# Kernel optimization log

Measured on AMD Instinct MI355X. Metric: run time of the kernel, lower is better.

The kernel has to match this reference:

```python
import jax, jax.numpy as jnp
import numpy as np

THETA = jnp.array([1.0, -0.5, 0.25, -0.125, 0.0625], dtype=jnp.float32)
N_NODES = 100000
N_EDGES = 1600000
D_FEAT = 32


def setup_inputs() -> dict:
    key = jax.random.key(0)
    k1, k2, k3 = jax.random.split(key, 3)
    feat = jax.random.normal(k1, (N_NODES, D_FEAT), dtype=jnp.float32)
    src = jax.random.randint(k2, (N_EDGES,), 0, N_NODES, dtype=jnp.int64)
    dst = jax.random.randint(k3, (N_EDGES,), 0, N_NODES, dtype=jnp.int64)
    return {"feat": feat, "src": src, "dst": dst}


def reference(feat, src, dst):
    n = feat.shape[0]
    # in-degree per node (edges counted by destination), clamped to >= 1
    deg = jax.ops.segment_sum(jnp.ones(src.shape[0], dtype=feat.dtype), dst, num_segments=n)
    d_invsqrt = jnp.maximum(deg, 1.0) ** -0.5  # [N]
    d_invsqrt = d_invsqrt[:, None]             # [N, 1]

    def unn_laplacian(f):
        # f - D^-1/2 A D^-1/2 f, via gather-from-src, scatter-sum-to-dst
        scaled = f * d_invsqrt                                   # [N, d]
        agg = jax.ops.segment_sum(scaled[src], dst, num_segments=n)  # [N, d]
        return f - agg * d_invsqrt

    h = THETA[0] * feat
    f = feat
    for k in range(1, THETA.shape[0]):
        f = unn_laplacian(f)
        h = h + THETA[k] * f
    return h
```

## Files before the change

### kernel.cpp

```cpp
#include <hip/hip_runtime.h>
#include <hip/hip_fp16.h>

#define D 32
#define BSHIFT 8
#define BNODES 256
#define NB_MAX 512
#define CHUNK 4096
#define CTHREADS 512

union H8 {
    float4 f4;
    __half2 h2[4];
};

__global__ void cursor_init(int* __restrict__ bcursor, int nb, int cap) {
    int tid = threadIdx.x;
    if (tid < nb) bcursor[tid] = tid * cap;
}

__global__ void scatter_bucket(const int* __restrict__ src, const int* __restrict__ dst,
                               int* __restrict__ bcursor, unsigned int* __restrict__ staged,
                               int n_edges, int cap) {
    __shared__ int cnt[NB_MAX];
    __shared__ int sbase[NB_MAX];
    __shared__ int gbase[NB_MAX];
    __shared__ unsigned int stg[CHUNK];
    __shared__ unsigned short stgb[CHUNK];
    int tid = threadIdx.x;
    for (int j = tid; j < NB_MAX; j += CTHREADS) cnt[j] = 0;
    __syncthreads();
    int base = blockIdx.x * CHUNK;
    const int EPT = CHUNK / CTHREADS;
    int b8[EPT], r8[EPT], s8[EPT], d8[EPT];
    #pragma unroll
    for (int k = 0; k < EPT; ++k) {
        int i = base + k * CTHREADS + tid;
        if (i < n_edges) {
            int dv = dst[i];
            s8[k] = src[i];
            d8[k] = dv & (BNODES - 1);
            b8[k] = dv >> BSHIFT;
            r8[k] = atomicAdd(&cnt[b8[k]], 1);
        } else {
            b8[k] = -1;
        }
    }
    __syncthreads();
    int v = cnt[tid];
    sbase[tid] = v;
    __syncthreads();
    for (int off = 1; off < NB_MAX; off <<= 1) {
        int t = (tid >= off) ? sbase[tid - off] : 0;
        __syncthreads();
        sbase[tid] += t;
        __syncthreads();
    }
    int excl = sbase[tid] - v;
    __syncthreads();
    sbase[tid] = excl;
    gbase[tid] = v ? atomicAdd(&bcursor[tid], v) : 0;
    __syncthreads();
    #pragma unroll
    for (int k = 0; k < EPT; ++k) {
        if (b8[k] >= 0) {
            int p = sbase[b8[k]] + r8[k];
            stg[p] = ((unsigned)s8[k] << BSHIFT) | (unsigned)d8[k];
            stgb[p] = (unsigned short)b8[k];
        }
    }
    __syncthreads();
    int valid = n_edges - base;
    if (valid > CHUNK) valid = CHUNK;
    for (int j = tid; j < valid; j += CTHREADS) {
        int b = stgb[j];
        int idx = gbase[b] + (j - sbase[b]);
        if (idx < (b + 1) * cap)
            staged[idx] = stg[j];
    }
}

__global__ void bucket_finalize(const int* __restrict__ bcursor, const unsigned int* __restrict__ staged,
                                int cap, int* __restrict__ csr, int2* __restrict__ rowinfo,
                                float* __restrict__ dinv2, float* __restrict__ dsq,
                                const float* __restrict__ feat, __half* __restrict__ s0,
                                int n_nodes) {
    __shared__ int cnt[BNODES];
    __shared__ int scn[BNODES];
    __shared__ int cursor[BNODES];
    __shared__ float ldinv[BNODES];
    int tid = threadIdx.x;
    int b = blockIdx.x;
    int node0 = b << BSHIFT;
    int nn = n_nodes - node0;
    if (nn > BNODES) nn = BNODES;
    int base = b * cap;
    int m = bcursor[b] - base;
    if (m > cap) m = cap;
    if (tid < BNODES) cnt[tid] = 0;
    __syncthreads();
    for (int j = tid; j < m; j += CTHREADS)
        atomicAdd(&cnt[staged[base + j] & (BNODES - 1)], 1);
    __syncthreads();
    if (tid < BNODES) scn[tid] = cnt[tid];
    __syncthreads();
    for (int off = 1; off < BNODES; off <<= 1) {
        int t = 0;
        if (tid < BNODES && tid >= off) t = scn[tid - off];
        __syncthreads();
        if (tid < BNODES) scn[tid] += t;
        __syncthreads();
    }
    if (tid < BNODES) {
        int excl = scn[tid] - cnt[tid];
        cursor[tid] = excl;
        if (tid < nn) {
            int2 ri = {base + excl, base + excl + cnt[tid]};
            rowinfo[node0 + tid] = ri;
            float fd = (float)cnt[tid];
            fd = fd < 1.0f ? 1.0f : fd;
            float dn = rsqrtf(fd);
            ldinv[tid] = dn;
            dinv2[node0 + tid] = dn * dn;
            dsq[node0 + tid] = sqrtf(fd);
        }
    }
    __syncthreads();
    for (int j = tid; j < m; j += CTHREADS) {
        unsigned int p = staged[base + j];
        int d = p & (BNODES - 1);
        int pos = atomicAdd(&cursor[d], 1);
        csr[base + pos] = (int)(p >> BSHIFT);
    }
    int ntask = nn * 4;
    for (int t = tid; t < ntask; t += CTHREADS) {
        int nl = t >> 2;
        int q8 = (t & 3) << 3;
        float dn = ldinv[nl];
        size_t off = ((size_t)(node0 + nl) << 5) + q8;
        float4 a = *reinterpret_cast<const float4*>(&feat[off]);
        float4 bb = *reinterpret_cast<const float4*>(&feat[off + 4]);
        H8 o;
        o.h2[0] = __floats2half2_rn(a.x * dn, a.y * dn);
        o.h2[1] = __floats2half2_rn(a.z * dn, a.w * dn);
        o.h2[2] = __floats2half2_rn(bb.x * dn, bb.y * dn);
        o.h2[3] = __floats2half2_rn(bb.z * dn, bb.w * dn);
        *reinterpret_cast<float4*>(&s0[off]) = o.f4;
    }
}

__device__ __forceinline__ void acc_row(const __half* __restrict__ s_cur, int sn, int q8,
                                        float& a0, float& a1, float& a2, float& a3,
                                        float& a4, float& a5, float& a6, float& a7) {
    H8 u;
    u.f4 = *reinterpret_cast<const float4*>(&s_cur[((size_t)sn << 5) + q8]);
    float2 p0 = __half22float2(u.h2[0]);
    float2 p1 = __half22float2(u.h2[1]);
    float2 p2 = __half22float2(u.h2[2]);
    float2 p3 = __half22float2(u.h2[3]);
    a0 += p0.x; a1 += p0.y; a2 += p1.x; a3 += p1.y;
    a4 += p2.x; a5 += p2.y; a6 += p3.x; a7 += p3.y;
}

__global__ void hop_kernel(const int2* __restrict__ rowinfo, const int* __restrict__ csr,
                           const float* __restrict__ dinv2, const __half* __restrict__ s_cur,
                           __half* __restrict__ s_next, int n_nodes) {
    int t = blockIdx.x * blockDim.x + threadIdx.x;
    int node = t >> 2;
    if (node >= n_nodes) return;
    int q8 = (t & 3) << 3;
    int2 ri = rowinfo[node];
    int e = ri.x, end = ri.y;
    float a0 = 0.f, a1 = 0.f, a2 = 0.f, a3 = 0.f, a4 = 0.f, a5 = 0.f, a6 = 0.f, a7 = 0.f;
    for (; e + 3 < end; e += 4) {
        int s0 = csr[e], s1 = csr[e + 1], s2 = csr[e + 2], s3 = csr[e + 3];
        acc_row(s_cur, s0, q8, a0, a1, a2, a3, a4, a5, a6, a7);
        acc_row(s_cur, s1, q8, a0, a1, a2, a3, a4, a5, a6, a7);
        acc_row(s_cur, s2, q8, a0, a1, a2, a3, a4, a5, a6, a7);
        acc_row(s_cur, s3, q8, a0, a1, a2, a3, a4, a5, a6, a7);
    }
    for (; e < end; ++e)
        acc_row(s_cur, csr[e], q8, a0, a1, a2, a3, a4, a5, a6, a7);
    size_t off = ((size_t)node << 5) + q8;
    float dn2 = dinv2[node];
    H8 sc;
    sc.f4 = *reinterpret_cast<const float4*>(&s_cur[off]);
    float2 c0 = __half22float2(sc.h2[0]);
    float2 c1 = __half22float2(sc.h2[1]);
    float2 c2 = __half22float2(sc.h2[2]);
    float2 c3 = __half22float2(sc.h2[3]);
    H8 so;
    so.h2[0] = __floats2half2_rn(c0.x - a0 * dn2, c0.y - a1 * dn2);
    so.h2[1] = __floats2half2_rn(c1.x - a2 * dn2, c1.y - a3 * dn2);
    so.h2[2] = __floats2half2_rn(c2.x - a4 * dn2, c2.y - a5 * dn2);
    so.h2[3] = __floats2half2_rn(c3.x - a6 * dn2, c3.y - a7 * dn2);
    *reinterpret_cast<float4*>(&s_next[off]) = so.f4;
}

__global__ void hop_last_kernel(const int2* __restrict__ rowinfo, const int* __restrict__ csr,
                                const float* __restrict__ dinv2, const float* __restrict__ dsq,
                                const __half* __restrict__ s1, const __half* __restrict__ s2,
                                const __half* __restrict__ s3, const float* __restrict__ feat,
                                float* __restrict__ h, int n_nodes) {
    int t = blockIdx.x * blockDim.x + threadIdx.x;
    int node = t >> 2;
    if (node >= n_nodes) return;
    int q8 = (t & 3) << 3;
    int2 ri = rowinfo[node];
    int e = ri.x, end = ri.y;
    float a0 = 0.f, a1 = 0.f, a2 = 0.f, a3 = 0.f, a4 = 0.f, a5 = 0.f, a6 = 0.f, a7 = 0.f;
    for (; e + 3 < end; e += 4) {
        int t0 = csr[e], t1 = csr[e + 1], t2 = csr[e + 2], t3 = csr[e + 3];
        acc_row(s3, t0, q8, a0, a1, a2, a3, a4, a5, a6, a7);
        acc_row(s3, t1, q8, a0, a1, a2, a3, a4, a5, a6, a7);
        acc_row(s3, t2, q8, a0, a1, a2, a3, a4, a5, a6, a7);
        acc_row(s3, t3, q8, a0, a1, a2, a3, a4, a5, a6, a7);
    }
    for (; e < end; ++e)
        acc_row(s3, csr[e], q8, a0, a1, a2, a3, a4, a5, a6, a7);
    size_t off = ((size_t)node << 5) + q8;
    float dn2 = dinv2[node];
    float ds = dsq[node];
    H8 u1, u2, u3;
    u1.f4 = *reinterpret_cast<const float4*>(&s1[off]);
    u2.f4 = *reinterpret_cast<const float4*>(&s2[off]);
    u3.f4 = *reinterpret_cast<const float4*>(&s3[off]);
    float4 fa = *reinterpret_cast<const float4*>(&feat[off]);
    float4 fb = *reinterpret_cast<const float4*>(&feat[off + 4]);
    const float th1 = -0.5f, th2 = 0.25f, th3 = -0.125f, th4 = 0.0625f;
    float r[8] = {fa.x, fa.y, fa.z, fa.w, fb.x, fb.y, fb.z, fb.w};
    float aa[8] = {a0, a1, a2, a3, a4, a5, a6, a7};
    #pragma unroll
    for (int j = 0; j < 4; ++j) {
        float2 p1 = __half22float2(u1.h2[j]);
        float2 p2 = __half22float2(u2.h2[j]);
        float2 p3 = __half22float2(u3.h2[j]);
        float s4x = p3.x - aa[2 * j] * dn2;
        float s4y = p3.y - aa[2 * j + 1] * dn2;
        float mx = fmaf(th1, p1.x, fmaf(th2, p2.x, fmaf(th3, p3.x, th4 * s4x)));
        float my = fmaf(th1, p1.y, fmaf(th2, p2.y, fmaf(th3, p3.y, th4 * s4y)));
        r[2 * j]     = fmaf(ds, mx, r[2 * j]);
        r[2 * j + 1] = fmaf(ds, my, r[2 * j + 1]);
    }
    float4 o0 = {r[0], r[1], r[2], r[3]};
    float4 o1 = {r[4], r[5], r[6], r[7]};
    *reinterpret_cast<float4*>(&h[off]) = o0;
    *reinterpret_cast<float4*>(&h[off + 4]) = o1;
}

extern "C" void kernel_launch(void* const* d_in, const int* in_sizes, int n_in,
                              void* d_out, int out_size, void* d_ws, size_t ws_size,
                              hipStream_t stream) {
    const float* feat = (const float*)d_in[0];
    const int*   src  = (const int*)d_in[1];
    const int*   dst  = (const int*)d_in[2];
    float* h = (float*)d_out;

    int n_nodes = in_sizes[0] / D;
    int n_edges = in_sizes[1];
    long long total_nf = (long long)n_nodes * D;
    int nb = (n_nodes + BNODES - 1) >> BSHIFT;
    int cap = (int)(((2LL * n_edges / nb) + 1023) & ~1023LL);

    char* w = (char*)d_ws;
    auto alloc = [&](size_t bytes) {
        char* p = w;
        w += (bytes + 15) & ~(size_t)15;
        return (void*)p;
    };
    int*          bcursor = (int*)alloc(NB_MAX * 4);
    int2*         rowinfo = (int2*)alloc((size_t)n_nodes * 8);
    unsigned int* staged  = (unsigned int*)alloc((size_t)nb * cap * 4);
    int*          csr     = (int*)alloc((size_t)nb * cap * 4);
    float*        dinv2   = (float*)alloc((size_t)n_nodes * 4);
    float*        dsq     = (float*)alloc((size_t)n_nodes * 4);
    __half*       s[4];
    for (int k = 0; k < 4; ++k) s[k] = (__half*)alloc((size_t)total_nf * 2);

    cursor_init<<<1, NB_MAX, 0, stream>>>(bcursor, nb, cap);
    int eblocks = (n_edges + CHUNK - 1) / CHUNK;
    scatter_bucket<<<eblocks, CTHREADS, 0, stream>>>(src, dst, bcursor, staged, n_edges, cap);
    bucket_finalize<<<nb, CTHREADS, 0, stream>>>(bcursor, staged, cap, csr, rowinfo,
                                                 dinv2, dsq, feat, s[0], n_nodes);

    int hop_threads = n_nodes * 4;
    int hop_blocks = (hop_threads + 255) / 256;
    for (int k = 1; k < 4; ++k)
        hop_kernel<<<hop_blocks, 256, 0, stream>>>(rowinfo, csr, dinv2, s[k - 1], s[k], n_nodes);
    hop_last_kernel<<<hop_blocks, 256, 0, stream>>>(rowinfo, csr, dinv2, dsq,
                                                    s[1], s[2], s[3], feat, h, n_nodes);
}
```

Measured before the change: 134.4 us.

## Sort nodes by degree within buckets, pack per-node metadata, unroll gathers by eight

Within each 256-node bucket, nodes are counting-sorted by in-degree into a permutation, so hop kernels process nodes of similar degree together and wavefront divergence from uneven neighbour loops drops. Row bounds, D^-1 and sqrt(D) are packed into one float4 per node, so each thread does one metadata load instead of several. The gather loop is unrolled to eight rows with all loads issued before the adds, giving more memory requests in flight. The cost is an extra indirection through perm, scattered output writes, and higher register pressure.

```diff
diff --git a/kernel.cpp b/kernel.cpp
--- a/kernel.cpp
+++ b/kernel.cpp
@@ -80,14 +80,15 @@
 }
 
 __global__ void bucket_finalize(const int* __restrict__ bcursor, const unsigned int* __restrict__ staged,
-                                int cap, int* __restrict__ csr, int2* __restrict__ rowinfo,
-                                float* __restrict__ dinv2, float* __restrict__ dsq,
-                                const float* __restrict__ feat, __half* __restrict__ s0,
-                                int n_nodes) {
+                                int cap, int* __restrict__ csr, float4* __restrict__ meta,
+                                int* __restrict__ perm, const float* __restrict__ feat,
+                                __half* __restrict__ s0, int n_nodes) {
     __shared__ int cnt[BNODES];
     __shared__ int scn[BNODES];
     __shared__ int cursor[BNODES];
     __shared__ float ldinv[BNODES];
+    __shared__ int dhist[64];
+    __shared__ int dcur[64];
     int tid = threadIdx.x;
     int b = blockIdx.x;
     int node0 = b << BSHIFT;
@@ -114,15 +115,40 @@
         int excl = scn[tid] - cnt[tid];
         cursor[tid] = excl;
         if (tid < nn) {
-            int2 ri = {base + excl, base + excl + cnt[tid]};
-            rowinfo[node0 + tid] = ri;
             float fd = (float)cnt[tid];
             fd = fd < 1.0f ? 1.0f : fd;
             float dn = rsqrtf(fd);
             ldinv[tid] = dn;
-            dinv2[node0 + tid] = dn * dn;
-            dsq[node0 + tid] = sqrtf(fd);
+            float4 mt;
+            mt.x = __int_as_float(base + excl);
+            mt.y = __int_as_float(base + excl + cnt[tid]);
+            mt.z = dn * dn;
+            mt.w = sqrtf(fd);
+            meta[node0 + tid] = mt;
         }
+    }
+    if (tid < 64) dhist[tid] = 0;
+    __syncthreads();
+    if (tid < nn) {
+        int dg = cnt[tid]; if (dg > 63) dg = 63;
+        atomicAdd(&dhist[dg], 1);
+    }
+    __syncthreads();
+    if (tid < 64) dcur[tid] = dhist[tid];
+    __syncthreads();
+    for (int off = 1; off < 64; off <<= 1) {
+        int t = 0;
+        if (tid < 64 && tid >= off) t = dcur[tid - off];
+        __syncthreads();
+        if (tid < 64) dcur[tid] += t;
+        __syncthreads();
+    }
+    if (tid < 64) dcur[tid] -= dhist[tid];
+    __syncthreads();
+    if (tid < nn) {
+        int dg = cnt[tid]; if (dg > 63) dg = 63;
+        int slot = atomicAdd(&dcur[dg], 1);
+        perm[node0 + slot] = node0 + tid;
     }
     __syncthreads();
     for (int j = tid; j < m; j += CTHREADS) {
@@ -148,40 +174,50 @@
     }
 }
 
-__device__ __forceinline__ void acc_row(const __half* __restrict__ s_cur, int sn, int q8,
-                                        float& a0, float& a1, float& a2, float& a3,
-                                        float& a4, float& a5, float& a6, float& a7) {
-    H8 u;
-    u.f4 = *reinterpret_cast<const float4*>(&s_cur[((size_t)sn << 5) + q8]);
-    float2 p0 = __half22float2(u.h2[0]);
-    float2 p1 = __half22float2(u.h2[1]);
-    float2 p2 = __half22float2(u.h2[2]);
-    float2 p3 = __half22float2(u.h2[3]);
-    a0 += p0.x; a1 += p0.y; a2 += p1.x; a3 += p1.y;
-    a4 += p2.x; a5 += p2.y; a6 += p3.x; a7 += p3.y;
-}
-
-__global__ void hop_kernel(const int2* __restrict__ rowinfo, const int* __restrict__ csr,
-                           const float* __restrict__ dinv2, const __half* __restrict__ s_cur,
+#define LDROW(U, IDX) (U).f4 = *reinterpret_cast<const float4*>(&tab[((size_t)(IDX) << 5) + q8])
+#define ADD8(U) { \
+    float2 p0 = __half22float2((U).h2[0]); \
+    float2 p1 = __half22float2((U).h2[1]); \
+    float2 p2 = __half22float2((U).h2[2]); \
+    float2 p3 = __half22float2((U).h2[3]); \
+    a0 += p0.x; a1 += p0.y; a2 += p1.x; a3 += p1.y; \
+    a4 += p2.x; a5 += p2.y; a6 += p3.x; a7 += p3.y; }
+
+__global__ void hop_kernel(const int* __restrict__ perm, const float4* __restrict__ meta,
+                           const int* __restrict__ csr, const __half* __restrict__ s_cur,
                            __half* __restrict__ s_next, int n_nodes) {
     int t = blockIdx.x * blockDim.x + threadIdx.x;
-    int node = t >> 2;
-    if (node >= n_nodes) return;
+    int ni = t >> 2;
+    if (ni >= n_nodes) return;
+    int node = perm[ni];
     int q8 = (t & 3) << 3;
-    int2 ri = rowinfo[node];
-    int e = ri.x, end = ri.y;
+    float4 mt = meta[node];
+    int e = __float_as_int(mt.x), end = __float_as_int(mt.y);
+    const __half* __restrict__ tab = s_cur;
     float a0 = 0.f, a1 = 0.f, a2 = 0.f, a3 = 0.f, a4 = 0.f, a5 = 0.f, a6 = 0.f, a7 = 0.f;
-    for (; e + 3 < end; e += 4) {
-        int s0 = csr[e], s1 = csr[e + 1], s2 = csr[e + 2], s3 = csr[e + 3];
-        acc_row(s_cur, s0, q8, a0, a1, a2, a3, a4, a5, a6, a7);
-        acc_row(s_cur, s1, q8, a0, a1, a2, a3, a4, a5, a6, a7);
-        acc_row(s_cur, s2, q8, a0, a1, a2, a3, a4, a5, a6, a7);
-        acc_row(s_cur, s3, q8, a0, a1, a2, a3, a4, a5, a6, a7);
-    }
-    for (; e < end; ++e)
-        acc_row(s_cur, csr[e], q8, a0, a1, a2, a3, a4, a5, a6, a7);
+    for (; e + 7 < end; e += 8) {
+        int i0 = csr[e],     i1 = csr[e + 1], i2 = csr[e + 2], i3 = csr[e + 3];
+        int i4 = csr[e + 4], i5 = csr[e + 5], i6 = csr[e + 6], i7 = csr[e + 7];
+        H8 u0, u1, u2, u3, u4, u5, u6, u7;
+        LDROW(u0, i0); LDROW(u1, i1); LDROW(u2, i2); LDROW(u3, i3);
+        LDROW(u4, i4); LDROW(u5, i5); LDROW(u6, i6); LDROW(u7, i7);
+        ADD8(u0); ADD8(u1); ADD8(u2); ADD8(u3);
+        ADD8(u4); ADD8(u5); ADD8(u6); ADD8(u7);
+    }
+    if (e + 3 < end) {
+        int i0 = csr[e], i1 = csr[e + 1], i2 = csr[e + 2], i3 = csr[e + 3];
+        H8 u0, u1, u2, u3;
+        LDROW(u0, i0); LDROW(u1, i1); LDROW(u2, i2); LDROW(u3, i3);
+        ADD8(u0); ADD8(u1); ADD8(u2); ADD8(u3);
+        e += 4;
+    }
+    for (; e < end; ++e) {
+        H8 u0;
+        LDROW(u0, csr[e]);
+        ADD8(u0);
+    }
     size_t off = ((size_t)node << 5) + q8;
-    float dn2 = dinv2[node];
+    float dn2 = mt.z;
     H8 sc;
     sc.f4 = *reinterpret_cast<const float4*>(&s_cur[off]);
     float2 c0 = __half22float2(sc.h2[0]);
@@ -196,30 +232,44 @@
     *reinterpret_cast<float4*>(&s_next[off]) = so.f4;
 }
 
-__global__ void hop_last_kernel(const int2* __restrict__ rowinfo, const int* __restrict__ csr,
-                                const float* __restrict__ dinv2, const float* __restrict__ dsq,
+__global__ void hop_last_kernel(const int* __restrict__ perm, const float4* __restrict__ meta,
+                                const int* __restrict__ csr,
                                 const __half* __restrict__ s1, const __half* __restrict__ s2,
                                 const __half* __restrict__ s3, const float* __restrict__ feat,
                                 float* __restrict__ h, int n_nodes) {
     int t = blockIdx.x * blockDim.x + threadIdx.x;
-    int node = t >> 2;
-    if (node >= n_nodes) return;
+    int ni = t >> 2;
+    if (ni >= n_nodes) return;
+    int node = perm[ni];
     int q8 = (t & 3) << 3;
-    int2 ri = rowinfo[node];
-    int e = ri.x, end = ri.y;
+    float4 mt = meta[node];
+    int e = __float_as_int(mt.x), end = __float_as_int(mt.y);
+    const __half* __restrict__ tab = s3;
     float a0 = 0.f, a1 = 0.f, a2 = 0.f, a3 = 0.f, a4 = 0.f, a5 = 0.f, a6 = 0.f, a7 = 0.f;
-    for (; e + 3 < end; e += 4) {
-        int t0 = csr[e], t1 = csr[e + 1], t2 = csr[e + 2], t3 = csr[e + 3];
-        acc_row(s3, t0, q8, a0, a1, a2, a3, a4, a5, a6, a7);
-        acc_row(s3, t1, q8, a0, a1, a2, a3, a4, a5, a6, a7);
-        acc_row(s3, t2, q8, a0, a1, a2, a3, a4, a5, a6, a7);
-        acc_row(s3, t3, q8, a0, a1, a2, a3, a4, a5, a6, a7);
-    }
-    for (; e < end; ++e)
-        acc_row(s3, csr[e], q8, a0, a1, a2, a3, a4, a5, a6, a7);
+    for (; e + 7 < end; e += 8) {
+        int i0 = csr[e],     i1 = csr[e + 1], i2 = csr[e + 2], i3 = csr[e + 3];
+        int i4 = csr[e + 4], i5 = csr[e + 5], i6 = csr[e + 6], i7 = csr[e + 7];
+        H8 u0, u1, u2, u3, u4, u5, u6, u7;
+        LDROW(u0, i0); LDROW(u1, i1); LDROW(u2, i2); LDROW(u3, i3);
+        LDROW(u4, i4); LDROW(u5, i5); LDROW(u6, i6); LDROW(u7, i7);
+        ADD8(u0); ADD8(u1); ADD8(u2); ADD8(u3);
+        ADD8(u4); ADD8(u5); ADD8(u6); ADD8(u7);
+    }
+    if (e + 3 < end) {
+        int i0 = csr[e], i1 = csr[e + 1], i2 = csr[e + 2], i3 = csr[e + 3];
+        H8 u0, u1, u2, u3;
+        LDROW(u0, i0); LDROW(u1, i1); LDROW(u2, i2); LDROW(u3, i3);
+        ADD8(u0); ADD8(u1); ADD8(u2); ADD8(u3);
+        e += 4;
+    }
+    for (; e < end; ++e) {
+        H8 u0;
+        LDROW(u0, csr[e]);
+        ADD8(u0);
+    }
     size_t off = ((size_t)node << 5) + q8;
-    float dn2 = dinv2[node];
-    float ds = dsq[node];
+    float dn2 = mt.z;
+    float ds = mt.w;
     H8 u1, u2, u3;
     u1.f4 = *reinterpret_cast<const float4*>(&s1[off]);
     u2.f4 = *reinterpret_cast<const float4*>(&s2[off]);
@@ -268,24 +318,23 @@
         return (void*)p;
     };
     int*          bcursor = (int*)alloc(NB_MAX * 4);
-    int2*         rowinfo = (int2*)alloc((size_t)n_nodes * 8);
+    float4*       meta    = (float4*)alloc((size_t)n_nodes * 16);
+    int*          perm    = (int*)alloc((size_t)n_nodes * 4);
     unsigned int* staged  = (unsigned int*)alloc((size_t)nb * cap * 4);
     int*          csr     = (int*)alloc((size_t)nb * cap * 4);
-    float*        dinv2   = (float*)alloc((size_t)n_nodes * 4);
-    float*        dsq     = (float*)alloc((size_t)n_nodes * 4);
     __half*       s[4];
     for (int k = 0; k < 4; ++k) s[k] = (__half*)alloc((size_t)total_nf * 2);
 
     cursor_init<<<1, NB_MAX, 0, stream>>>(bcursor, nb, cap);
     int eblocks = (n_edges + CHUNK - 1) / CHUNK;
     scatter_bucket<<<eblocks, CTHREADS, 0, stream>>>(src, dst, bcursor, staged, n_edges, cap);
-    bucket_finalize<<<nb, CTHREADS, 0, stream>>>(bcursor, staged, cap, csr, rowinfo,
-                                                 dinv2, dsq, feat, s[0], n_nodes);
+    bucket_finalize<<<nb, CTHREADS, 0, stream>>>(bcursor, staged, cap, csr, meta,
+                                                 perm, feat, s[0], n_nodes);
 
     int hop_threads = n_nodes * 4;
     int hop_blocks = (hop_threads + 255) / 256;
     for (int k = 1; k < 4; ++k)
-        hop_kernel<<<hop_blocks, 256, 0, stream>>>(rowinfo, csr, dinv2, s[k - 1], s[k], n_nodes);
-    hop_last_kernel<<<hop_blocks, 256, 0, stream>>>(rowinfo, csr, dinv2, dsq,
+        hop_kernel<<<hop_blocks, 256, 0, stream>>>(perm, meta, csr, s[k - 1], s[k], n_nodes);
+    hop_last_kernel<<<hop_blocks, 256, 0, stream>>>(perm, meta, csr,
                                                     s[1], s[2], s[3], feat, h, n_nodes);
 }
```

Measured after the change: 159.9 us. 1.19x slower.

## Split half-precision feature table into two 16-column planes processed per launch

Applied to the files above, without the earlier changes.

The fp16 scaled-feature table is reorganised into two planar halves of 16 columns each, and every hop runs as two launches, one per half. Within a half, pairs of threads split the edge list and combine their partial sums with a lane shuffle. The goal is a smaller gather working set per launch, for better cache hit rates, plus more parallelism per node. Per-node metadata (row range, dinv², sqrt deg) is packed into one float4, and nontemporal loads and stores are used for CSR indices and outputs. In exchange, the CSR index list is read twice per hop, there are twice as many launches, and half the threads sit idle during the epilogue.

```diff
diff --git a/kernel.cpp b/kernel.cpp
--- a/kernel.cpp
+++ b/kernel.cpp
@@ -8,8 +8,11 @@
 #define CHUNK 4096
 #define CTHREADS 512
 
+typedef float vf4 __attribute__((ext_vector_type(4)));
+
 union H8 {
     float4 f4;
+    vf4 v4;
     __half2 h2[4];
 };
 
@@ -80,8 +83,7 @@
 }
 
 __global__ void bucket_finalize(const int* __restrict__ bcursor, const unsigned int* __restrict__ staged,
-                                int cap, int* __restrict__ csr, int2* __restrict__ rowinfo,
-                                float* __restrict__ dinv2, float* __restrict__ dsq,
+                                int cap, int* __restrict__ csr, float4* __restrict__ meta,
                                 const float* __restrict__ feat, __half* __restrict__ s0,
                                 int n_nodes) {
     __shared__ int cnt[BNODES];
@@ -114,14 +116,16 @@
         int excl = scn[tid] - cnt[tid];
         cursor[tid] = excl;
         if (tid < nn) {
-            int2 ri = {base + excl, base + excl + cnt[tid]};
-            rowinfo[node0 + tid] = ri;
             float fd = (float)cnt[tid];
             fd = fd < 1.0f ? 1.0f : fd;
             float dn = rsqrtf(fd);
             ldinv[tid] = dn;
-            dinv2[node0 + tid] = dn * dn;
-            dsq[node0 + tid] = sqrtf(fd);
+            float4 mt;
+            mt.x = __int_as_float(base + excl);
+            mt.y = __int_as_float(base + excl + cnt[tid]);
+            mt.z = dn * dn;
+            mt.w = sqrtf(fd);
+            meta[node0 + tid] = mt;
         }
     }
     __syncthreads();
@@ -134,117 +138,129 @@
     int ntask = nn * 4;
     for (int t = tid; t < ntask; t += CTHREADS) {
         int nl = t >> 2;
-        int q8 = (t & 3) << 3;
+        int p = (t >> 1) & 1;
+        int q8 = (t & 1) << 3;
         float dn = ldinv[nl];
-        size_t off = ((size_t)(node0 + nl) << 5) + q8;
-        float4 a = *reinterpret_cast<const float4*>(&feat[off]);
-        float4 bb = *reinterpret_cast<const float4*>(&feat[off + 4]);
+        int node = node0 + nl;
+        const float* fsrc = &feat[(size_t)node * D + p * 16 + q8];
+        float4 a = *reinterpret_cast<const float4*>(fsrc);
+        float4 bb = *reinterpret_cast<const float4*>(fsrc + 4);
         H8 o;
         o.h2[0] = __floats2half2_rn(a.x * dn, a.y * dn);
         o.h2[1] = __floats2half2_rn(a.z * dn, a.w * dn);
         o.h2[2] = __floats2half2_rn(bb.x * dn, bb.y * dn);
         o.h2[3] = __floats2half2_rn(bb.z * dn, bb.w * dn);
-        *reinterpret_cast<float4*>(&s0[off]) = o.f4;
-    }
-}
-
-__device__ __forceinline__ void acc_row(const __half* __restrict__ s_cur, int sn, int q8,
-                                        float& a0, float& a1, float& a2, float& a3,
-                                        float& a4, float& a5, float& a6, float& a7) {
-    H8 u;
-    u.f4 = *reinterpret_cast<const float4*>(&s_cur[((size_t)sn << 5) + q8]);
-    float2 p0 = __half22float2(u.h2[0]);
-    float2 p1 = __half22float2(u.h2[1]);
-    float2 p2 = __half22float2(u.h2[2]);
-    float2 p3 = __half22float2(u.h2[3]);
-    a0 += p0.x; a1 += p0.y; a2 += p1.x; a3 += p1.y;
-    a4 += p2.x; a5 += p2.y; a6 += p3.x; a7 += p3.y;
-}
-
-__global__ void hop_kernel(const int2* __restrict__ rowinfo, const int* __restrict__ csr,
-                           const float* __restrict__ dinv2, const __half* __restrict__ s_cur,
-                           __half* __restrict__ s_next, int n_nodes) {
+        *reinterpret_cast<float4*>(&s0[(((size_t)p * n_nodes + node) << 4) + q8]) = o.f4;
+    }
+}
+
+#define LDROW16(U, IDX) (U).f4 = *reinterpret_cast<const float4*>(&tab[((size_t)(IDX) << 4) + q8])
+#define ADD8(U) { \
+    float2 p0 = __half22float2((U).h2[0]); \
+    float2 p1 = __half22float2((U).h2[1]); \
+    float2 p2 = __half22float2((U).h2[2]); \
+    float2 p3 = __half22float2((U).h2[3]); \
+    a0 += p0.x; a1 += p0.y; a2 += p1.x; a3 += p1.y; \
+    a4 += p2.x; a5 += p2.y; a6 += p3.x; a7 += p3.y; }
+
+#define GATHER_LOOP(TAB) \
+    int e = start + sub; \
+    for (; e + 6 < end; e += 8) { \
+        int i0 = __builtin_nontemporal_load(&csr[e]); \
+        int i1 = __builtin_nontemporal_load(&csr[e + 2]); \
+        int i2 = __builtin_nontemporal_load(&csr[e + 4]); \
+        int i3 = __builtin_nontemporal_load(&csr[e + 6]); \
+        H8 u0, u1, u2, u3; \
+        const __half* __restrict__ tab = (TAB); \
+        LDROW16(u0, i0); LDROW16(u1, i1); LDROW16(u2, i2); LDROW16(u3, i3); \
+        ADD8(u0); ADD8(u1); ADD8(u2); ADD8(u3); \
+    } \
+    for (; e < end; e += 2) { \
+        H8 u0; \
+        const __half* __restrict__ tab = (TAB); \
+        LDROW16(u0, __builtin_nontemporal_load(&csr[e])); \
+        ADD8(u0); \
+    } \
+    a0 += __shfl_xor(a0, 2, 64); a1 += __shfl_xor(a1, 2, 64); \
+    a2 += __shfl_xor(a2, 2, 64); a3 += __shfl_xor(a3, 2, 64); \
+    a4 += __shfl_xor(a4, 2, 64); a5 += __shfl_xor(a5, 2, 64); \
+    a6 += __shfl_xor(a6, 2, 64); a7 += __shfl_xor(a7, 2, 64);
+
+__global__ void hop_half(const float4* __restrict__ meta, const int* __restrict__ csr,
+                         const __half* __restrict__ s_cur, __half* __restrict__ s_next,
+                         int n_nodes) {
     int t = blockIdx.x * blockDim.x + threadIdx.x;
     int node = t >> 2;
     if (node >= n_nodes) return;
-    int q8 = (t & 3) << 3;
-    int2 ri = rowinfo[node];
-    int e = ri.x, end = ri.y;
+    int sub = (t >> 1) & 1;
+    int q8 = (t & 1) << 3;
+    float4 mt = meta[node];
+    int start = __float_as_int(mt.x), end = __float_as_int(mt.y);
     float a0 = 0.f, a1 = 0.f, a2 = 0.f, a3 = 0.f, a4 = 0.f, a5 = 0.f, a6 = 0.f, a7 = 0.f;
-    for (; e + 3 < end; e += 4) {
-        int s0 = csr[e], s1 = csr[e + 1], s2 = csr[e + 2], s3 = csr[e + 3];
-        acc_row(s_cur, s0, q8, a0, a1, a2, a3, a4, a5, a6, a7);
-        acc_row(s_cur, s1, q8, a0, a1, a2, a3, a4, a5, a6, a7);
-        acc_row(s_cur, s2, q8, a0, a1, a2, a3, a4, a5, a6, a7);
-        acc_row(s_cur, s3, q8, a0, a1, a2, a3, a4, a5, a6, a7);
-    }
-    for (; e < end; ++e)
-        acc_row(s_cur, csr[e], q8, a0, a1, a2, a3, a4, a5, a6, a7);
-    size_t off = ((size_t)node << 5) + q8;
-    float dn2 = dinv2[node];
-    H8 sc;
-    sc.f4 = *reinterpret_cast<const float4*>(&s_cur[off]);
-    float2 c0 = __half22float2(sc.h2[0]);
-    float2 c1 = __half22float2(sc.h2[1]);
-    float2 c2 = __half22float2(sc.h2[2]);
-    float2 c3 = __half22float2(sc.h2[3]);
-    H8 so;
-    so.h2[0] = __floats2half2_rn(c0.x - a0 * dn2, c0.y - a1 * dn2);
-    so.h2[1] = __floats2half2_rn(c1.x - a2 * dn2, c1.y - a3 * dn2);
-    so.h2[2] = __floats2half2_rn(c2.x - a4 * dn2, c2.y - a5 * dn2);
-    so.h2[3] = __floats2half2_rn(c3.x - a6 * dn2, c3.y - a7 * dn2);
-    *reinterpret_cast<float4*>(&s_next[off]) = so.f4;
-}
-
-__global__ void hop_last_kernel(const int2* __restrict__ rowinfo, const int* __restrict__ csr,
-                                const float* __restrict__ dinv2, const float* __restrict__ dsq,
-                                const __half* __restrict__ s1, const __half* __restrict__ s2,
-                                const __half* __restrict__ s3, const float* __restrict__ feat,
-                                float* __restrict__ h, int n_nodes) {
+    GATHER_LOOP(s_cur)
+    if (sub == 0) {
+        size_t off = ((size_t)node << 4) + q8;
+        float dn2 = mt.z;
+        H8 sc;
+        sc.f4 = *reinterpret_cast<const float4*>(&s_cur[off]);
+        float2 c0 = __half22float2(sc.h2[0]);
+        float2 c1 = __half22float2(sc.h2[1]);
+        float2 c2 = __half22float2(sc.h2[2]);
+        float2 c3 = __half22float2(sc.h2[3]);
+        H8 so;
+        so.h2[0] = __floats2half2_rn(c0.x - a0 * dn2, c0.y - a1 * dn2);
+        so.h2[1] = __floats2half2_rn(c1.x - a2 * dn2, c1.y - a3 * dn2);
+        so.h2[2] = __floats2half2_rn(c2.x - a4 * dn2, c2.y - a5 * dn2);
+        so.h2[3] = __floats2half2_rn(c3.x - a6 * dn2, c3.y - a7 * dn2);
+        __builtin_nontemporal_store(so.v4, reinterpret_cast<vf4*>(&s_next[off]));
+    }
+}
+
+__global__ void hop_last_half(const float4* __restrict__ meta, const int* __restrict__ csr,
+                              const __half* __restrict__ s1, const __half* __restrict__ s2,
+                              const __half* __restrict__ s3, const float* __restrict__ feat,
+                              float* __restrict__ h, int p, int n_nodes) {
     int t = blockIdx.x * blockDim.x + threadIdx.x;
     int node = t >> 2;
     if (node >= n_nodes) return;
-    int q8 = (t & 3) << 3;
-    int2 ri = rowinfo[node];
-    int e = ri.x, end = ri.y;
+    int sub = (t >> 1) & 1;
+    int q8 = (t & 1) << 3;
+    float4 mt = meta[node];
+    int start = __float_as_int(mt.x), end = __float_as_int(mt.y);
     float a0 = 0.f, a1 = 0.f, a2 = 0.f, a3 = 0.f, a4 = 0.f, a5 = 0.f, a6 = 0.f, a7 = 0.f;
-    for (; e + 3 < end; e += 4) {
-        int t0 = csr[e], t1 = csr[e + 1], t2 = csr[e + 2], t3 = csr[e + 3];
-        acc_row(s3, t0, q8, a0, a1, a2, a3, a4, a5, a6, a7);
-        acc_row(s3, t1, q8, a0, a1, a2, a3, a4, a5, a6, a7);
-        acc_row(s3, t2, q8, a0, a1, a2, a3, a4, a5, a6, a7);
-        acc_row(s3, t3, q8, a0, a1, a2, a3, a4, a5, a6, a7);
-    }
-    for (; e < end; ++e)
-        acc_row(s3, csr[e], q8, a0, a1, a2, a3, a4, a5, a6, a7);
-    size_t off = ((size_t)node << 5) + q8;
-    float dn2 = dinv2[node];
-    float ds = dsq[node];
-    H8 u1, u2, u3;
-    u1.f4 = *reinterpret_cast<const float4*>(&s1[off]);
-    u2.f4 = *reinterpret_cast<const float4*>(&s2[off]);
-    u3.f4 = *reinterpret_cast<const float4*>(&s3[off]);
-    float4 fa = *reinterpret_cast<const float4*>(&feat[off]);
-    float4 fb = *reinterpret_cast<const float4*>(&feat[off + 4]);
-    const float th1 = -0.5f, th2 = 0.25f, th3 = -0.125f, th4 = 0.0625f;
-    float r[8] = {fa.x, fa.y, fa.z, fa.w, fb.x, fb.y, fb.z, fb.w};
-    float aa[8] = {a0, a1, a2, a3, a4, a5, a6, a7};
-    #pragma unroll
-    for (int j = 0; j < 4; ++j) {
-        float2 p1 = __half22float2(u1.h2[j]);
-        float2 p2 = __half22float2(u2.h2[j]);
-        float2 p3 = __half22float2(u3.h2[j]);
-        float s4x = p3.x - aa[2 * j] * dn2;
-        float s4y = p3.y - aa[2 * j + 1] * dn2;
-        float mx = fmaf(th1, p1.x, fmaf(th2, p2.x, fmaf(th3, p3.x, th4 * s4x)));
-        float my = fmaf(th1, p1.y, fmaf(th2, p2.y, fmaf(th3, p3.y, th4 * s4y)));
-        r[2 * j]     = fmaf(ds, mx, r[2 * j]);
-        r[2 * j + 1] = fmaf(ds, my, r[2 * j + 1]);
-    }
-    float4 o0 = {r[0], r[1], r[2], r[3]};
-    float4 o1 = {r[4], r[5], r[6], r[7]};
-    *reinterpret_cast<float4*>(&h[off]) = o0;
-    *reinterpret_cast<float4*>(&h[off + 4]) = o1;
+    GATHER_LOOP(s3)
+    if (sub == 0) {
+        size_t off = ((size_t)node << 4) + q8;
+        float dn2 = mt.z;
+        float ds = mt.w;
+        H8 u1, u2, u3;
+        u1.f4 = *reinterpret_cast<const float4*>(&s1[off]);
+        u2.f4 = *reinterpret_cast<const float4*>(&s2[off]);
+        u3.f4 = *reinterpret_cast<const float4*>(&s3[off]);
+        const float* fsrc = &feat[(size_t)node * D + p * 16 + q8];
+        float4 fa = *reinterpret_cast<const float4*>(fsrc);
+        float4 fb = *reinterpret_cast<const float4*>(fsrc + 4);
+        const float th1 = -0.5f, th2 = 0.25f, th3 = -0.125f, th4 = 0.0625f;
+        float r[8] = {fa.x, fa.y, fa.z, fa.w, fb.x, fb.y, fb.z, fb.w};
+        float aa[8] = {a0, a1, a2, a3, a4, a5, a6, a7};
+        #pragma unroll
+        for (int j = 0; j < 4; ++j) {
+            float2 p1 = __half22float2(u1.h2[j]);
+            float2 p2 = __half22float2(u2.h2[j]);
+            float2 p3 = __half22float2(u3.h2[j]);
+            float s4x = p3.x - aa[2 * j] * dn2;
+            float s4y = p3.y - aa[2 * j + 1] * dn2;
+            float mx = fmaf(th1, p1.x, fmaf(th2, p2.x, fmaf(th3, p3.x, th4 * s4x)));
+            float my = fmaf(th1, p1.y, fmaf(th2, p2.y, fmaf(th3, p3.y, th4 * s4y)));
+            r[2 * j]     = fmaf(ds, mx, r[2 * j]);
+            r[2 * j + 1] = fmaf(ds, my, r[2 * j + 1]);
+        }
+        float* hdst = &h[(size_t)node * D + p * 16 + q8];
+        vf4 o0 = {r[0], r[1], r[2], r[3]};
+        vf4 o1 = {r[4], r[5], r[6], r[7]};
+        __builtin_nontemporal_store(o0, reinterpret_cast<vf4*>(hdst));
+        __builtin_nontemporal_store(o1, reinterpret_cast<vf4*>(hdst + 4));
+    }
 }
 
 extern "C" void kernel_launch(void* const* d_in, const int* in_sizes, int n_in,
@@ -268,24 +284,30 @@
         return (void*)p;
     };
     int*          bcursor = (int*)alloc(NB_MAX * 4);
-    int2*         rowinfo = (int2*)alloc((size_t)n_nodes * 8);
+    float4*       meta    = (float4*)alloc((size_t)n_nodes * 16);
     unsigned int* staged  = (unsigned int*)alloc((size_t)nb * cap * 4);
     int*          csr     = (int*)alloc((size_t)nb * cap * 4);
-    float*        dinv2   = (float*)alloc((size_t)n_nodes * 4);
-    float*        dsq     = (float*)alloc((size_t)n_nodes * 4);
     __half*       s[4];
     for (int k = 0; k < 4; ++k) s[k] = (__half*)alloc((size_t)total_nf * 2);
+    size_t hstride = (size_t)n_nodes * 16;
 
     cursor_init<<<1, NB_MAX, 0, stream>>>(bcursor, nb, cap);
     int eblocks = (n_edges + CHUNK - 1) / CHUNK;
     scatter_bucket<<<eblocks, CTHREADS, 0, stream>>>(src, dst, bcursor, staged, n_edges, cap);
-    bucket_finalize<<<nb, CTHREADS, 0, stream>>>(bcursor, staged, cap, csr, rowinfo,
-                                                 dinv2, dsq, feat, s[0], n_nodes);
+    bucket_finalize<<<nb, CTHREADS, 0, stream>>>(bcursor, staged, cap, csr, meta,
+                                                 feat, s[0], n_nodes);
 
     int hop_threads = n_nodes * 4;
     int hop_blocks = (hop_threads + 255) / 256;
     for (int k = 1; k < 4; ++k)
-        hop_kernel<<<hop_blocks, 256, 0, stream>>>(rowinfo, csr, dinv2, s[k - 1], s[k], n_nodes);
-    hop_last_kernel<<<hop_blocks, 256, 0, stream>>>(rowinfo, csr, dinv2, dsq,
-                                                    s[1], s[2], s[3], feat, h, n_nodes);
-}
+        for (int p = 0; p < 2; ++p)
+            hop_half<<<hop_blocks, 256, 0, stream>>>(meta, csr,
+                                                     s[k - 1] + p * hstride,
+                                                     s[k] + p * hstride, n_nodes);
+    for (int p = 0; p < 2; ++p)
+        hop_last_half<<<hop_blocks, 256, 0, stream>>>(meta, csr,
+                                                      s[1] + p * hstride,
+                                                      s[2] + p * hstride,
+                                                      s[3] + p * hstride,
+                                                      feat, h, p, n_nodes);
+}
```

After: 211.7 us. +57.5%, slower.
